# Optimization experiments

Measured on AMD Instinct MI355X. Metric: run time of the kernel, lower is better.

The kernel has to match this reference:

```python
import jax, jax.numpy as jnp
import numpy as np

EPS = 1e-5

def spmm(rows, cols, vals, x, n_out):
    # COO sparse [n_out, n_in] @ x [n_in, d] -> [n_out, d]
    return jax.ops.segment_sum(vals[:, None] * x[cols], rows, num_segments=n_out)

def layernorm(x, g, b):
    mu = jnp.mean(x, axis=-1, keepdims=True)
    var = jnp.var(x, axis=-1, keepdims=True)
    return (x - mu) * jax.lax.rsqrt(var + EPS) * g + b

def setup_inputs() -> dict:
    key = jax.random.key(0)
    ks = jax.random.split(key, 32)
    N, D = 100000, 512
    N0, N1, N2 = 131072, 32768, 8192
    E_s0, E_s1 = 262144, 65536
    E_f0, E_f1 = 1048576, 262144
    s = 1.0 / np.sqrt(D)
    inp = {
        'x': jax.random.normal(ks[0], (N, D), jnp.float32),
        'hist0': jax.random.normal(ks[1], (N, D), jnp.float32),
        'hist1': jax.random.normal(ks[2], (N, D), jnp.float32),
        'w0': jax.random.normal(ks[3], (D, D), jnp.float32) * s,
        'b0': jax.random.normal(ks[4], (D,), jnp.float32) * s,
        'g0': jnp.ones((D,), jnp.float32),
        'beta0': jnp.zeros((D,), jnp.float32),
        'w1': jax.random.normal(ks[5], (D, D), jnp.float32) * s,
        'b1': jax.random.normal(ks[6], (D,), jnp.float32) * s,
        'sadj0_vals': jax.random.uniform(ks[7], (E_s0,), jnp.float32),
        'sadj1_vals': jax.random.uniform(ks[8], (E_s1,), jnp.float32),
        'fadj0_vals': jax.random.uniform(ks[9], (E_f0,), jnp.float32),
        'fadj1_vals': jax.random.uniform(ks[10], (E_f1,), jnp.float32),
        'sid0': jax.random.randint(ks[11], (N0,), 0, N),
        'sid1': jax.random.randint(ks[12], (N1,), 0, N),
        'sid2': jax.random.randint(ks[13], (N2,), 0, N),
        'fid0': jax.random.randint(ks[14], (N0,), 0, N),
        'fid1': jax.random.randint(ks[15], (N1,), 0, N),
        'sadj0_rows': jax.random.randint(ks[16], (E_s0,), 0, N1),
        'sadj0_cols': jax.random.randint(ks[17], (E_s0,), 0, N0),
        'sadj1_rows': jax.random.randint(ks[18], (E_s1,), 0, N2),
        'sadj1_cols': jax.random.randint(ks[19], (E_s1,), 0, N1),
        'fadj0_rows': jax.random.randint(ks[20], (E_f0,), 0, N1),
        'fadj0_cols': jax.random.randint(ks[21], (E_f0,), 0, N0),
        'fadj1_rows': jax.random.randint(ks[22], (E_f1,), 0, N2),
        'fadj1_cols': jax.random.randint(ks[23], (E_f1,), 0, N1),
    }
    return inp

def reference(x, hist0, hist1, w0, b0, g0, beta0, w1, b1,
              sadj0_vals, sadj1_vals, fadj0_vals, fadj1_vals,
              sid0, sid1, sid2, fid0, fid1,
              sadj0_rows, sadj0_cols, sadj1_rows, sadj1_cols,
              fadj0_rows, fadj0_cols, fadj1_rows, fadj1_cols):
    N1 = sid1.shape[0]
    N2 = sid2.shape[0]
    sg = jax.lax.stop_gradient
    # layer 0
    h = x[sid0]                                   # [N0, D]
    h = h - sg(hist0[sid0])                        # variance-reduction correction
    full = sg(spmm(fadj0_rows, fadj0_cols, fadj0_vals, hist0[fid0], N1))
    h = spmm(sadj0_rows, sadj0_cols, sadj0_vals, h, N1) + full  # [N1, D]
    h = h @ w0.T + b0
    h = jax.nn.relu(layernorm(h, g0, beta0))
    # layer 1 (last: no norm/relu)
    h = h - sg(hist1[sid1])
    full = sg(spmm(fadj1_rows, fadj1_cols, fadj1_vals, hist1[fid1], N2))
    h = spmm(sadj1_rows, sadj1_cols, sadj1_vals, h, N2) + full  # [N2, D]
    h = h @ w1.T + b1
    return jax.nn.log_softmax(h, axis=-1)
```

## Files before the change

### kernel.cpp

```cpp
#include <hip/hip_runtime.h>

#define D 512
#define NTAB 100000

typedef __bf16 bf16x8 __attribute__((ext_vector_type(8)));
typedef float f32x4 __attribute__((ext_vector_type(4)));
typedef float f32x2 __attribute__((ext_vector_type(2)));

__device__ __forceinline__ unsigned f2bf(float f){
  union { float f; unsigned u; } v; v.f = f;
  unsigned r = v.u + 0x7fffu + ((v.u >> 16) & 1u);
  return r >> 16;
}
__device__ __forceinline__ float bf2f(unsigned h){
  union { unsigned u; float f; } v; v.u = h << 16; return v.f;
}
__device__ __forceinline__ uint2 enc_fp8x8(f32x4 v0, f32x4 v1){
  int lo = __builtin_amdgcn_cvt_pk_fp8_f32(v0[0], v0[1], 0, false);
  lo     = __builtin_amdgcn_cvt_pk_fp8_f32(v0[2], v0[3], lo, true);
  int hi = __builtin_amdgcn_cvt_pk_fp8_f32(v1[0], v1[1], 0, false);
  hi     = __builtin_amdgcn_cvt_pk_fp8_f32(v1[2], v1[3], hi, true);
  return make_uint2((unsigned)lo, (unsigned)hi);
}

#define MA_NS   6400
#define MA_GRID (MA_NS*9 + 512)

__global__ __launch_bounds__(256) void k_megaA(
    const int* __restrict__ s0r, int nS0,
    const int* __restrict__ f0r, int nF0, int* __restrict__ cnt0,
    const int* __restrict__ s1r, int nS1, int* __restrict__ cnt_s1,
    const int* __restrict__ f1r, int nF1, int* __restrict__ cnt_f1,
    const float* __restrict__ x, const float* __restrict__ hist0,
    unsigned char* __restrict__ T0q,
    const float* __restrict__ w0, const float* __restrict__ w1,
    unsigned short* __restrict__ w0b, unsigned short* __restrict__ w1b)
{
  int b = blockIdx.x, t = threadIdx.x;
  if (b < MA_NS*9){
    int sb = b / 9, r = b % 9;
    if (r == 0){
      int i = sb*256 + t;
      if (i < nS0){ atomicAdd(&cnt0[s0r[i]], 2); return; }
      i -= nS0;
      if (i < nF0){ atomicAdd(&cnt0[f0r[i]], 1); return; }
      i -= nF0;
      if (i < nS1){ atomicAdd(&cnt_s1[s1r[i]], 1); return; }
      i -= nS1;
      atomicAdd(&cnt_f1[f1r[i]], 1);
      return;
    }
    int ci = (sb*8 + (r-1))*256 + t;
    const int PER = NTAB*D/8;
    if (ci >= 2*PER) return;
    const float* src = (ci < PER) ? x : hist0;
    int ii = (ci < PER) ? ci : ci - PER;
    const f32x4* p = (const f32x4*)(src + (size_t)ii*8);
    f32x4 v0 = __builtin_nontemporal_load(p);
    f32x4 v1 = __builtin_nontemporal_load(p+1);
    *(uint2*)(T0q + (size_t)ci*8) = enc_fp8x8(v0, v1);
  } else {
    int i = (b - MA_NS*9)*256 + t;
    const float* src = (i < 65536) ? w0 : w1;
    unsigned short* dst = (i < 65536) ? w0b : w1b;
    int ii = (i < 65536) ? i : i - 65536;
    f32x4 v = *(const f32x4*)(src + (size_t)ii*4);
    ushort4 o;
    o.x = (unsigned short)f2bf(v[0]); o.y = (unsigned short)f2bf(v[1]);
    o.z = (unsigned short)f2bf(v[2]); o.w = (unsigned short)f2bf(v[3]);
    *(ushort4*)(dst + (size_t)ii*4) = o;
  }
}

__global__ __launch_bounds__(1024) void k_exscan3(
    const int* c0, int* r0, int n0,
    const int* c1, int* r1, int n1,
    const int* c2, int* r2, int n2)
{
  __shared__ int part[1024];
  const int* cnt; int* rp; int n;
  switch (blockIdx.x){
    case 0: cnt=c0; rp=r0; n=n0; break;
    case 1: cnt=c1; rp=r1; n=n1; break;
    default: cnt=c2; rp=r2; n=n2; break;
  }
  int t = threadIdx.x;
  int chunk = n >> 10;
  int base = t*chunk;
  int s = 0;
  for (int i=0;i<chunk;i++) s += cnt[base+i];
  part[t] = s; __syncthreads();
  for (int off=1; off<1024; off<<=1){
    int v = (t>=off) ? part[t-off] : 0;
    __syncthreads();
    part[t] += v;
    __syncthreads();
  }
  int run = (t==0) ? 0 : part[t-1];
  for (int i=0;i<chunk;i++){ rp[base+i] = run; run += cnt[base+i]; }
  if (t == 1023) rp[n] = run;
}

#define MB_NS   6554
#define MB_GRID (MB_NS*6)

__global__ __launch_bounds__(256) void k_megaB(
    const int* __restrict__ s0r, const int* __restrict__ s0c, const float* __restrict__ s0v, int nS0,
    const int* __restrict__ f0r, const int* __restrict__ f0c, const float* __restrict__ f0v, int nF0,
    const int* __restrict__ sid0, const int* __restrict__ fid0,
    const int* __restrict__ rp0, int* __restrict__ fill0, int2* __restrict__ bce0,
    const int* __restrict__ s1r, const int* __restrict__ s1c, const float* __restrict__ s1v, int nS1,
    const int* __restrict__ rp_s1, int* __restrict__ fill_s1, int2* __restrict__ bce_s1,
    const int* __restrict__ f1r, const int* __restrict__ f1c, const float* __restrict__ f1v, int nF1,
    const int* __restrict__ rp_f1, int* __restrict__ fill_f1, int2* __restrict__ bce_f1,
    const float* __restrict__ hist1, const int* __restrict__ fid1, const int* __restrict__ sid1,
    unsigned short* __restrict__ g1buf, unsigned short* __restrict__ s1buf)
{
  int b = blockIdx.x, t = threadIdx.x;
  int sb = b / 6, r = b % 6;
  if (r == 0){
    if (sb >= 6400) return;
    int i = sb*256 + t;
    if (i < nS0){
      int rr = s0r[i];
      int p = atomicAdd(&fill0[rr], 2);
      int base = rp0[rr] + p;
      int c = sid0[s0c[i]];
      float v = s0v[i];
      bce0[base]   = make_int2(c,        __float_as_int(v));
      bce0[base+1] = make_int2(NTAB + c, __float_as_int(-v));
      return;
    }
    i -= nS0;
    if (i < nF0){
      int rr = f0r[i];
      int p = atomicAdd(&fill0[rr], 1);
      bce0[rp0[rr] + p] = make_int2(NTAB + fid0[f0c[i]], __float_as_int(f0v[i]));
      return;
    }
    i -= nF0;
    if (i < nS1){
      int rr = s1r[i];
      int p = atomicAdd(&fill_s1[rr], 1);
      bce_s1[rp_s1[rr] + p] = make_int2(s1c[i], __float_as_int(s1v[i]));
      return;
    }
    i -= nS1;
    {
      int rr = f1r[i];
      int p = atomicAdd(&fill_f1[rr], 1);
      bce_f1[rp_f1[rr] + p] = make_int2(f1c[i], __float_as_int(f1v[i]));
    }
  } else {
    int g = sb*5 + (r-1);
    if (g >= 32768) return;
    const int* idx = (g < 16384) ? fid1 : sid1;
    unsigned short* dst = (g < 16384) ? g1buf : s1buf;
    if (g >= 16384) g -= 16384;
    int gt = g*256 + t;
    int row = gt >> 7, q = (gt & 127) << 2;
    int s = idx[row];
    f32x4 v = __builtin_nontemporal_load((const f32x4*)(hist1 + (size_t)s*D + q));
    ushort4 o;
    o.x = (unsigned short)f2bf(v[0]); o.y = (unsigned short)f2bf(v[1]);
    o.z = (unsigned short)f2bf(v[2]); o.w = (unsigned short)f2bf(v[3]);
    *(ushort4*)(dst + (size_t)row*D + q) = o;
  }
}

__device__ __forceinline__ void acc_bf16(float* a, uint4 p, float v){
  a[0] += v*bf2f(p.x & 0xffffu); a[1] += v*bf2f(p.x >> 16);
  a[2] += v*bf2f(p.y & 0xffffu); a[3] += v*bf2f(p.y >> 16);
  a[4] += v*bf2f(p.z & 0xffffu); a[5] += v*bf2f(p.z >> 16);
  a[6] += v*bf2f(p.w & 0xffffu); a[7] += v*bf2f(p.w >> 16);
}
__device__ __forceinline__ void acc_fp8(float* a, uint2 q, float v){
  f32x2 d0 = __builtin_amdgcn_cvt_pk_f32_fp8(q.x, false);
  f32x2 d1 = __builtin_amdgcn_cvt_pk_f32_fp8(q.x, true);
  f32x2 d2 = __builtin_amdgcn_cvt_pk_f32_fp8(q.y, false);
  f32x2 d3 = __builtin_amdgcn_cvt_pk_f32_fp8(q.y, true);
  a[0] += v*d0[0]; a[1] += v*d0[1]; a[2] += v*d1[0]; a[3] += v*d1[1];
  a[4] += v*d2[0]; a[5] += v*d2[1]; a[6] += v*d3[0]; a[7] += v*d3[1];
}

__device__ __forceinline__ void spmm_phase(
    const int* __restrict__ rp, const int2* __restrict__ be,
    const unsigned short* __restrict__ H, int row, int lane, float* a)
{
  int j = rp[row], je = rp[row+1];
  for (; j + 8 <= je; j += 8){
    int2 e[8]; uint4 p[8];
    #pragma unroll
    for (int u=0;u<8;u++) e[u] = be[j+u];
    #pragma unroll
    for (int u=0;u<8;u++) p[u] = *(const uint4*)(H + (size_t)e[u].x*D + lane*8);
    #pragma unroll
    for (int u=0;u<8;u++) acc_bf16(a, p[u], __int_as_float(e[u].y));
  }
  if (j + 4 <= je){
    int2 e[4]; uint4 p[4];
    #pragma unroll
    for (int u=0;u<4;u++) e[u] = be[j+u];
    #pragma unroll
    for (int u=0;u<4;u++) p[u] = *(const uint4*)(H + (size_t)e[u].x*D + lane*8);
    #pragma unroll
    for (int u=0;u<4;u++) acc_bf16(a, p[u], __int_as_float(e[u].y));
    j += 4;
  }
  for (; j < je; j++){
    int2 e = be[j];
    uint4 p = *(const uint4*)(H + (size_t)e.x*D + lane*8);
    acc_bf16(a, p, __int_as_float(e.y));
  }
}

__device__ __forceinline__ void spmm_phase_q8(
    const int* __restrict__ rp, const int2* __restrict__ be,
    const unsigned char* __restrict__ Q, int row, int lane, float* a)
{
  int j = rp[row], je = rp[row+1];
  for (; j + 8 <= je; j += 8){
    int2 e[8]; uint2 q[8];
    #pragma unroll
    for (int u=0;u<8;u++) e[u] = be[j+u];
    #pragma unroll
    for (int u=0;u<8;u++) q[u] = *(const uint2*)(Q + (size_t)e[u].x*D + lane*8);
    #pragma unroll
    for (int u=0;u<8;u++) acc_fp8(a, q[u], __int_as_float(e[u].y));
  }
  if (j + 4 <= je){
    int2 e[4]; uint2 q[4];
    #pragma unroll
    for (int u=0;u<4;u++) e[u] = be[j+u];
    #pragma unroll
    for (int u=0;u<4;u++) q[u] = *(const uint2*)(Q + (size_t)e[u].x*D + lane*8);
    #pragma unroll
    for (int u=0;u<4;u++) acc_fp8(a, q[u], __int_as_float(e[u].y));
    j += 4;
  }
  for (; j < je; j++){
    int2 e = be[j];
    uint2 q = *(const uint2*)(Q + (size_t)e.x*D + lane*8);
    acc_fp8(a, q, __int_as_float(e.y));
  }
}

__device__ __forceinline__ void store_row(unsigned short* out, int row, int lane, const float* a){
  uint4 o;
  o.x = f2bf(a[0]) | (f2bf(a[1]) << 16);
  o.y = f2bf(a[2]) | (f2bf(a[3]) << 16);
  o.z = f2bf(a[4]) | (f2bf(a[5]) << 16);
  o.w = f2bf(a[6]) | (f2bf(a[7]) << 16);
  *(uint4*)(out + (size_t)row*D + lane*8) = o;
}

__global__ __launch_bounds__(256) void k_spmm0(
    const int* __restrict__ rp, const int2* __restrict__ be,
    const unsigned char* __restrict__ T0q,
    unsigned short* __restrict__ out, int nrows)
{
  int wid = threadIdx.x >> 6, lane = threadIdx.x & 63;
  int row = blockIdx.x*4 + wid;
  if (row >= nrows) return;
  float a[8] = {0.f,0.f,0.f,0.f,0.f,0.f,0.f,0.f};
  spmm_phase_q8(rp, be, T0q, row, lane, a);
  store_row(out, row, lane, a);
}

__global__ __launch_bounds__(256) void k_spmm_acc(
    const int* __restrict__ rp, const int2* __restrict__ be, const unsigned short* __restrict__ H,
    unsigned short* __restrict__ out, int nrows)
{
  int wid = threadIdx.x >> 6, lane = threadIdx.x & 63;
  int row = blockIdx.x*4 + wid;
  if (row >= nrows) return;
  float a[8];
  uint4 p = *(const uint4*)(out + (size_t)row*D + lane*8);
  a[0]=bf2f(p.x&0xffffu); a[1]=bf2f(p.x>>16); a[2]=bf2f(p.y&0xffffu); a[3]=bf2f(p.y>>16);
  a[4]=bf2f(p.z&0xffffu); a[5]=bf2f(p.z>>16); a[6]=bf2f(p.w&0xffffu); a[7]=bf2f(p.w>>16);
  spmm_phase(rp, be, H, row, lane, a);
  store_row(out, row, lane, a);
}

__device__ __forceinline__ void gload16(const unsigned short* g, unsigned short* l){
  __builtin_amdgcn_global_load_lds(
      (const __attribute__((address_space(1))) unsigned int*)(const void*)g,
      (__attribute__((address_space(3))) unsigned int*)(void*)l,
      16, 0, 0);
}

template<bool OUT_BF16>
__device__ __forceinline__ void gemm_block(
    const unsigned short* __restrict__ A,
    const unsigned short* __restrict__ B,
    const float* __restrict__ bias,
    void* __restrict__ Cv,
    int gemm_bid, unsigned short* Al, unsigned short* Bl)
{
  int bx = gemm_bid & 3, by = gemm_bid >> 2;
  int m0 = by << 7, n0 = bx << 7;
  int t = threadIdx.x, wave = t >> 6, lane = t & 63;
  int wr = wave >> 1, wc = wave & 1;
  f32x4 acc[4][4] = {};
  int flat = t << 3;
  int r0 = flat >> 5, cc = flat & 31;
  const unsigned short* pa = A + (size_t)(m0 + r0)*D + cc;
  const unsigned short* pb = B + (size_t)(n0 + r0)*D + cc;
  for (int k0 = 0; k0 < D; k0 += 32){
    gload16(pa + k0,                 &Al[flat]);
    gload16(pa + (size_t)64*D + k0,  &Al[flat + 2048]);
    gload16(pb + k0,                 &Bl[flat]);
    gload16(pb + (size_t)64*D + k0,  &Bl[flat + 2048]);
    __syncthreads();
    int arow = (wr << 6) | (lane & 15);
    int brow = (wc << 6) | (lane & 15);
    int kg   = (lane >> 4) << 3;
    bf16x8 af[4], bfr[4];
    #pragma unroll
    for (int mi=0; mi<4; mi++) af[mi]  = *(const bf16x8*)&Al[(arow + (mi<<4))*32 + kg];
    #pragma unroll
    for (int ni=0; ni<4; ni++) bfr[ni] = *(const bf16x8*)&Bl[(brow + (ni<<4))*32 + kg];
    #pragma unroll
    for (int mi=0; mi<4; mi++)
      #pragma unroll
      for (int ni=0; ni<4; ni++)
        acc[mi][ni] = __builtin_amdgcn_mfma_f32_16x16x32_bf16(af[mi], bfr[ni], acc[mi][ni], 0, 0, 0);
    __syncthreads();
  }
  int crow = m0 + (wr << 6) + ((lane >> 4) << 2);
  int ccol = n0 + (wc << 6) + (lane & 15);
  #pragma unroll
  for (int mi=0; mi<4; mi++){
    #pragma unroll
    for (int q=0; q<4; q++){
      int row = crow + (mi << 4) + q;
      #pragma unroll
      for (int ni=0; ni<4; ni++){
        float val = acc[mi][ni][q] + bias[ccol + (ni << 4)];
        if (OUT_BF16)
          ((unsigned short*)Cv)[(size_t)row*D + ccol + (ni << 4)] = (unsigned short)f2bf(val);
        else
          ((float*)Cv)[(size_t)row*D + ccol + (ni << 4)] = val;
      }
    }
  }
}

__global__ __launch_bounds__(256) void k_megaC(
    const unsigned short* __restrict__ A, const unsigned short* __restrict__ B,
    const float* __restrict__ bias, unsigned short* __restrict__ y1,
    const int* __restrict__ rpf, const int2* __restrict__ bef,
    const unsigned short* __restrict__ g1buf, unsigned short* __restrict__ out2, int n2rows)
{
  __shared__ unsigned short Al[128*32];
  __shared__ unsigned short Bl[128*32];
  int b = blockIdx.x, t = threadIdx.x;
  int sb = b / 3, r = b % 3;
  if (r == 0){
    gemm_block<true>(A, B, bias, (void*)y1, sb, Al, Bl);
  } else {
    int wid = t >> 6, lane = t & 63;
    int row = (sb*2 + (r-1))*4 + wid;
    if (row >= n2rows) return;
    float a[8] = {0.f,0.f,0.f,0.f,0.f,0.f,0.f,0.f};
    spmm_phase(rpf, bef, g1buf, row, lane, a);
    store_row(out2, row, lane, a);
  }
}

template<bool OUT_BF16>
__global__ __launch_bounds__(256) void k_gemm_bias(
    const unsigned short* __restrict__ A,
    const unsigned short* __restrict__ B,
    const float* __restrict__ bias,
    void* __restrict__ Cv,
    int M)
{
  __shared__ unsigned short Al[128*32];
  __shared__ unsigned short Bl[128*32];
  gemm_block<OUT_BF16>(A, B, bias, Cv, blockIdx.x, Al, Bl);
}

__global__ __launch_bounds__(256) void k_ln_relu_sub(
    const unsigned short* __restrict__ y, const float* __restrict__ gam, const float* __restrict__ bet,
    const unsigned short* __restrict__ s1buf, unsigned short* __restrict__ out)
{
  __shared__ float sh[8];
  int row = blockIdx.x, t = threadIdx.x;
  int c = t << 1;
  unsigned pv = *(const unsigned*)(y + (size_t)row*D + c);
  float vx = bf2f(pv & 0xffffu), vy = bf2f(pv >> 16);
  float s = vx + vy, ss = vx*vx + vy*vy;
  #pragma unroll
  for (int m=1; m<64; m<<=1){ s += __shfl_xor(s, m); ss += __shfl_xor(ss, m); }
  int wave = t >> 6, lane = t & 63;
  if (lane == 0){ sh[wave] = s; sh[4+wave] = ss; }
  __syncthreads();
  s  = sh[0]+sh[1]+sh[2]+sh[3];
  ss = sh[4]+sh[5]+sh[6]+sh[7];
  float mu  = s * (1.f/D);
  float var = ss * (1.f/D) - mu*mu;
  float rr  = rsqrtf(var + 1e-5f);
  unsigned hv = *(const unsigned*)(s1buf + (size_t)row*D + c);
  float o0 = fmaxf((vx - mu)*rr*gam[c]   + bet[c],   0.f) - bf2f(hv & 0xffffu);
  float o1 = fmaxf((vy - mu)*rr*gam[c+1] + bet[c+1], 0.f) - bf2f(hv >> 16);
  *(unsigned*)(out + (size_t)row*D + c) = f2bf(o0) | (f2bf(o1) << 16);
}

__global__ __launch_bounds__(256) void k_logsoftmax(const float* __restrict__ y, float* __restrict__ out){
  __shared__ float sh[8];
  int row = blockIdx.x, t = threadIdx.x;
  int c = t << 1;
  float2 v = *(const float2*)(y + (size_t)row*D + c);
  float m = fmaxf(v.x, v.y);
  #pragma unroll
  for (int k=1; k<64; k<<=1) m = fmaxf(m, __shfl_xor(m, k));
  int wave = t >> 6, lane = t & 63;
  if (lane == 0) sh[wave] = m;
  __syncthreads();
  m = fmaxf(fmaxf(sh[0], sh[1]), fmaxf(sh[2], sh[3]));
  __syncthreads();
  float e = expf(v.x - m) + expf(v.y - m);
  #pragma unroll
  for (int k=1; k<64; k<<=1) e += __shfl_xor(e, k);
  if (lane == 0) sh[4+wave] = e;
  __syncthreads();
  e = sh[4]+sh[5]+sh[6]+sh[7];
  float lse = m + logf(e);
  float2 o; o.x = v.x - lse; o.y = v.y - lse;
  *(float2*)(out + (size_t)row*D + c) = o;
}

extern "C" void kernel_launch(void* const* d_in, const int* in_sizes, int n_in,
                              void* d_out, int out_size, void* d_ws, size_t ws_size,
                              hipStream_t stream)
{
  const float* x     = (const float*)d_in[0];
  const float* hist0 = (const float*)d_in[1];
  const float* hist1 = (const float*)d_in[2];
  const float* w0    = (const float*)d_in[3];
  const float* b0    = (const float*)d_in[4];
  const float* g0    = (const float*)d_in[5];
  const float* beta0 = (const float*)d_in[6];
  const float* w1    = (const float*)d_in[7];
  const float* b1    = (const float*)d_in[8];
  const float* s0v   = (const float*)d_in[9];
  const float* s1v   = (const float*)d_in[10];
  const float* f0v   = (const float*)d_in[11];
  const float* f1v   = (const float*)d_in[12];
  const int* sid0    = (const int*)d_in[13];
  const int* sid1    = (const int*)d_in[14];
  const int* fid0    = (const int*)d_in[16];
  const int* fid1    = (const int*)d_in[17];
  const int* s0r     = (const int*)d_in[18];
  const int* s0c     = (const int*)d_in[19];
  const int* s1r     = (const int*)d_in[20];
  const int* s1c     = (const int*)d_in[21];
  const int* f0r     = (const int*)d_in[22];
  const int* f0c     = (const int*)d_in[23];
  const int* f1r     = (const int*)d_in[24];
  const int* f1c     = (const int*)d_in[25];

  const int N1 = 32768, N2 = 8192;
  const int Es0 = 262144, Es1 = 65536, Ef0 = 1048576, Ef1 = 262144;
  const int E0 = 2*Es0 + Ef0;

  char* ws = (char*)d_ws;
  size_t off = 0;
  auto alloc = [&](size_t bytes)->char*{
    char* p = ws + off; off += (bytes + 255) & ~(size_t)255; return p;
  };
  char* T0q_raw = alloc((size_t)2*NTAB*D);
  unsigned short* g1buf = (unsigned short*)alloc((size_t)N1*D*2);
  unsigned short* s1buf = (unsigned short*)alloc((size_t)N1*D*2);
  unsigned short* h1    = (unsigned short*)alloc((size_t)N1*D*2);
  unsigned short* out1  = (unsigned short*)alloc((size_t)N1*D*2);
  unsigned short* w0b   = (unsigned short*)alloc((size_t)D*D*2);
  unsigned short* w1b   = (unsigned short*)alloc((size_t)D*D*2);
  int* meta = (int*)alloc((size_t)(2*N1 + 4*N2)*4);
  int* cnt0   = meta;            int* fill0   = cnt0 + N1;
  int* cnt_s1 = fill0 + N1;      int* fill_s1 = cnt_s1 + N2;
  int* cnt_f1 = fill_s1 + N2;    int* fill_f1 = cnt_f1 + N2;
  size_t metaBytes = (size_t)(2*N1 + 4*N2)*4;
  int* rp0   = (int*)alloc((size_t)(N1+1)*4);
  int* rp_s1 = (int*)alloc((size_t)(N2+1)*4);
  int* rp_f1 = (int*)alloc((size_t)(N2+1)*4);
  int2* bce0   = (int2*)alloc((size_t)E0*8);
  int2* bce_s1 = (int2*)alloc((size_t)Es1*8);
  int2* bce_f1 = (int2*)alloc((size_t)Ef1*8);

  unsigned char*  T0q  = (unsigned char*)T0q_raw;
  unsigned short* y1   = (unsigned short*)T0q_raw;
  float*          y2   = (float*)(T0q_raw + ((size_t)34<<20));
  unsigned short* out2 = (unsigned short*)(T0q_raw + ((size_t)52<<20));
  float*          outp = (float*)d_out;

  hipMemsetAsync(meta, 0, metaBytes, stream);
  k_megaA<<<MA_GRID, 256, 0, stream>>>(
      s0r, Es0, f0r, Ef0, cnt0, s1r, Es1, cnt_s1, f1r, Ef1, cnt_f1,
      x, hist0, T0q, w0, w1, w0b, w1b);
  k_exscan3<<<3, 1024, 0, stream>>>(cnt0, rp0, N1, cnt_s1, rp_s1, N2, cnt_f1, rp_f1, N2);
  k_megaB<<<MB_GRID, 256, 0, stream>>>(
      s0r, s0c, s0v, Es0, f0r, f0c, f0v, Ef0, sid0, fid0, rp0, fill0, bce0,
      s1r, s1c, s1v, Es1, rp_s1, fill_s1, bce_s1,
      f1r, f1c, f1v, Ef1, rp_f1, fill_f1, bce_f1,
      hist1, fid1, sid1, g1buf, s1buf);
  k_spmm0<<<N1/4, 256, 0, stream>>>(rp0, bce0, T0q, out1, N1);
  k_megaC<<<1024*3, 256, 0, stream>>>(out1, w0b, b0, y1, rp_f1, bce_f1, g1buf, out2, N2);
  k_ln_relu_sub<<<N1, 256, 0, stream>>>(y1, g0, beta0, s1buf, h1);
  k_spmm_acc<<<N2/4, 256, 0, stream>>>(rp_s1, bce_s1, h1, out2, N2);
  k_gemm_bias<false><<<(N2/128)*4, 256, 0, stream>>>(out2, w1b, b1, (void*)y2, N2);
  k_logsoftmax<<<N2, 256, 0, stream>>>(y2, outp);
}
```

Measured before the change: 549.7 us.

## Quantize full hist1 table to fp8 and index it directly instead of gathering bf16 copies

hist1 is now converted whole into an fp8 table (H1q) inside the first mega kernel, replacing the per-row bf16 gathers into g1buf/s1buf. The fill kernel now stores fid1 indices in the f1 CSR entries, and the layernorm kernel reads H1q through sid1. This removes the separate gather-and-convert pass and shrinks the bytes read in the second-layer spmm and the subtraction. In exchange it converts all 100k rows of hist1 rather than only the 64k gathered ones, and fp8 loses precision compared with bf16. Numeric tolerance may be at risk.

```diff
diff --git a/kernel.cpp b/kernel.cpp
--- a/kernel.cpp
+++ b/kernel.cpp
@@ -24,21 +24,22 @@
 }
 
 #define MA_NS   6400
-#define MA_GRID (MA_NS*9 + 512)
+#define MA_GRID (MA_NS*13 + 512)
+#define PER8    (NTAB*D/8)
 
 __global__ __launch_bounds__(256) void k_megaA(
     const int* __restrict__ s0r, int nS0,
     const int* __restrict__ f0r, int nF0, int* __restrict__ cnt0,
     const int* __restrict__ s1r, int nS1, int* __restrict__ cnt_s1,
     const int* __restrict__ f1r, int nF1, int* __restrict__ cnt_f1,
-    const float* __restrict__ x, const float* __restrict__ hist0,
-    unsigned char* __restrict__ T0q,
+    const float* __restrict__ x, const float* __restrict__ hist0, const float* __restrict__ hist1,
+    unsigned char* __restrict__ T0q, unsigned char* __restrict__ H1q,
     const float* __restrict__ w0, const float* __restrict__ w1,
     unsigned short* __restrict__ w0b, unsigned short* __restrict__ w1b)
 {
   int b = blockIdx.x, t = threadIdx.x;
-  if (b < MA_NS*9){
-    int sb = b / 9, r = b % 9;
+  if (b < MA_NS*13){
+    int sb = b / 13, r = b % 13;
     if (r == 0){
       int i = sb*256 + t;
       if (i < nS0){ atomicAdd(&cnt0[s0r[i]], 2); return; }
@@ -50,17 +51,28 @@
       atomicAdd(&cnt_f1[f1r[i]], 1);
       return;
     }
-    int ci = (sb*8 + (r-1))*256 + t;
-    const int PER = NTAB*D/8;
-    if (ci >= 2*PER) return;
-    const float* src = (ci < PER) ? x : hist0;
-    int ii = (ci < PER) ? ci : ci - PER;
-    const f32x4* p = (const f32x4*)(src + (size_t)ii*8);
-    f32x4 v0 = __builtin_nontemporal_load(p);
-    f32x4 v1 = __builtin_nontemporal_load(p+1);
-    *(uint2*)(T0q + (size_t)ci*8) = enc_fp8x8(v0, v1);
+    if (r < 9){
+      int ci = (sb*8 + (r-1))*256 + t;
+      if (ci >= 2*PER8) return;
+      const float* src = (ci < PER8) ? x : hist0;
+      int ii = (ci < PER8) ? ci : ci - PER8;
+      const f32x4* p = (const f32x4*)(src + (size_t)ii*8);
+      f32x4 v0 = __builtin_nontemporal_load(p);
+      f32x4 v1 = __builtin_nontemporal_load(p+1);
+      *(uint2*)(T0q + (size_t)ci*8) = enc_fp8x8(v0, v1);
+      return;
+    }
+    {
+      int ci = (sb*4 + (r-9))*256 + t;
+      if (ci >= PER8) return;
+      const f32x4* p = (const f32x4*)(hist1 + (size_t)ci*8);
+      f32x4 v0 = __builtin_nontemporal_load(p);
+      f32x4 v1 = __builtin_nontemporal_load(p+1);
+      *(uint2*)(H1q + (size_t)ci*8) = enc_fp8x8(v0, v1);
+      return;
+    }
   } else {
-    int i = (b - MA_NS*9)*256 + t;
+    int i = (b - MA_NS*13)*256 + t;
     const float* src = (i < 65536) ? w0 : w1;
     unsigned short* dst = (i < 65536) ? w0b : w1b;
     int ii = (i < 65536) ? i : i - 65536;
@@ -101,70 +113,49 @@
   if (t == 1023) rp[n] = run;
 }
 
-#define MB_NS   6554
-#define MB_GRID (MB_NS*6)
-
-__global__ __launch_bounds__(256) void k_megaB(
+__global__ __launch_bounds__(256) void k_fill(
     const int* __restrict__ s0r, const int* __restrict__ s0c, const float* __restrict__ s0v, int nS0,
     const int* __restrict__ f0r, const int* __restrict__ f0c, const float* __restrict__ f0v, int nF0,
     const int* __restrict__ sid0, const int* __restrict__ fid0,
     const int* __restrict__ rp0, int* __restrict__ fill0, int2* __restrict__ bce0,
     const int* __restrict__ s1r, const int* __restrict__ s1c, const float* __restrict__ s1v, int nS1,
     const int* __restrict__ rp_s1, int* __restrict__ fill_s1, int2* __restrict__ bce_s1,
-    const int* __restrict__ f1r, const int* __restrict__ f1c, const float* __restrict__ f1v, int nF1,
-    const int* __restrict__ rp_f1, int* __restrict__ fill_f1, int2* __restrict__ bce_f1,
-    const float* __restrict__ hist1, const int* __restrict__ fid1, const int* __restrict__ sid1,
-    unsigned short* __restrict__ g1buf, unsigned short* __restrict__ s1buf)
-{
-  int b = blockIdx.x, t = threadIdx.x;
-  int sb = b / 6, r = b % 6;
-  if (r == 0){
-    if (sb >= 6400) return;
-    int i = sb*256 + t;
-    if (i < nS0){
-      int rr = s0r[i];
-      int p = atomicAdd(&fill0[rr], 2);
-      int base = rp0[rr] + p;
-      int c = sid0[s0c[i]];
-      float v = s0v[i];
-      bce0[base]   = make_int2(c,        __float_as_int(v));
-      bce0[base+1] = make_int2(NTAB + c, __float_as_int(-v));
-      return;
-    }
-    i -= nS0;
-    if (i < nF0){
-      int rr = f0r[i];
-      int p = atomicAdd(&fill0[rr], 1);
-      bce0[rp0[rr] + p] = make_int2(NTAB + fid0[f0c[i]], __float_as_int(f0v[i]));
-      return;
-    }
-    i -= nF0;
-    if (i < nS1){
-      int rr = s1r[i];
-      int p = atomicAdd(&fill_s1[rr], 1);
-      bce_s1[rp_s1[rr] + p] = make_int2(s1c[i], __float_as_int(s1v[i]));
-      return;
-    }
-    i -= nS1;
-    {
-      int rr = f1r[i];
-      int p = atomicAdd(&fill_f1[rr], 1);
-      bce_f1[rp_f1[rr] + p] = make_int2(f1c[i], __float_as_int(f1v[i]));
-    }
-  } else {
-    int g = sb*5 + (r-1);
-    if (g >= 32768) return;
-    const int* idx = (g < 16384) ? fid1 : sid1;
-    unsigned short* dst = (g < 16384) ? g1buf : s1buf;
-    if (g >= 16384) g -= 16384;
-    int gt = g*256 + t;
-    int row = gt >> 7, q = (gt & 127) << 2;
-    int s = idx[row];
-    f32x4 v = __builtin_nontemporal_load((const f32x4*)(hist1 + (size_t)s*D + q));
-    ushort4 o;
-    o.x = (unsigned short)f2bf(v[0]); o.y = (unsigned short)f2bf(v[1]);
-    o.z = (unsigned short)f2bf(v[2]); o.w = (unsigned short)f2bf(v[3]);
-    *(ushort4*)(dst + (size_t)row*D + q) = o;
+    const int* __restrict__ f1r, const int* __restrict__ f1c, const float* __restrict__ f1v,
+    const int* __restrict__ fid1,
+    const int* __restrict__ rp_f1, int* __restrict__ fill_f1, int2* __restrict__ bce_f1)
+{
+  int i = blockIdx.x*256 + threadIdx.x;
+  if (i < nS0){
+    int rr = s0r[i];
+    int c  = sid0[s0c[i]];
+    float v = s0v[i];
+    int p = atomicAdd(&fill0[rr], 2);
+    int base = rp0[rr] + p;
+    bce0[base]   = make_int2(c,        __float_as_int(v));
+    bce0[base+1] = make_int2(NTAB + c, __float_as_int(-v));
+    return;
+  }
+  i -= nS0;
+  if (i < nF0){
+    int rr = f0r[i];
+    int c  = NTAB + fid0[f0c[i]];
+    int p = atomicAdd(&fill0[rr], 1);
+    bce0[rp0[rr] + p] = make_int2(c, __float_as_int(f0v[i]));
+    return;
+  }
+  i -= nF0;
+  if (i < nS1){
+    int rr = s1r[i];
+    int p = atomicAdd(&fill_s1[rr], 1);
+    bce_s1[rp_s1[rr] + p] = make_int2(s1c[i], __float_as_int(s1v[i]));
+    return;
+  }
+  i -= nS1;
+  {
+    int rr = f1r[i];
+    int c  = fid1[f1c[i]];
+    int p = atomicAdd(&fill_f1[rr], 1);
+    bce_f1[rp_f1[rr] + p] = make_int2(c, __float_as_int(f1v[i]));
   }
 }
 
@@ -350,7 +341,7 @@
     const unsigned short* __restrict__ A, const unsigned short* __restrict__ B,
     const float* __restrict__ bias, unsigned short* __restrict__ y1,
     const int* __restrict__ rpf, const int2* __restrict__ bef,
-    const unsigned short* __restrict__ g1buf, unsigned short* __restrict__ out2, int n2rows)
+    const unsigned char* __restrict__ H1q, unsigned short* __restrict__ out2, int n2rows)
 {
   __shared__ unsigned short Al[128*32];
   __shared__ unsigned short Bl[128*32];
@@ -363,7 +354,7 @@
     int row = (sb*2 + (r-1))*4 + wid;
     if (row >= n2rows) return;
     float a[8] = {0.f,0.f,0.f,0.f,0.f,0.f,0.f,0.f};
-    spmm_phase(rpf, bef, g1buf, row, lane, a);
+    spmm_phase_q8(rpf, bef, H1q, row, lane, a);
     store_row(out2, row, lane, a);
   }
 }
@@ -381,9 +372,10 @@
   gemm_block<OUT_BF16>(A, B, bias, Cv, blockIdx.x, Al, Bl);
 }
 
-__global__ __launch_bounds__(256) void k_ln_relu_sub(
+__global__ __launch_bounds__(256) void k_ln_relu_subq(
     const unsigned short* __restrict__ y, const float* __restrict__ gam, const float* __restrict__ bet,
-    const unsigned short* __restrict__ s1buf, unsigned short* __restrict__ out)
+    const unsigned char* __restrict__ H1q, const int* __restrict__ sid1,
+    unsigned short* __restrict__ out)
 {
   __shared__ float sh[8];
   int row = blockIdx.x, t = threadIdx.x;
@@ -401,9 +393,11 @@
   float mu  = s * (1.f/D);
   float var = ss * (1.f/D) - mu*mu;
   float rr  = rsqrtf(var + 1e-5f);
-  unsigned hv = *(const unsigned*)(s1buf + (size_t)row*D + c);
-  float o0 = fmaxf((vx - mu)*rr*gam[c]   + bet[c],   0.f) - bf2f(hv & 0xffffu);
-  float o1 = fmaxf((vy - mu)*rr*gam[c+1] + bet[c+1], 0.f) - bf2f(hv >> 16);
+  int srow = sid1[row];
+  unsigned short qv = *(const unsigned short*)(H1q + (size_t)srow*D + c);
+  f32x2 d = __builtin_amdgcn_cvt_pk_f32_fp8((unsigned)qv, false);
+  float o0 = fmaxf((vx - mu)*rr*gam[c]   + bet[c],   0.f) - d[0];
+  float o1 = fmaxf((vy - mu)*rr*gam[c+1] + bet[c+1], 0.f) - d[1];
   *(unsigned*)(out + (size_t)row*D + c) = f2bf(o0) | (f2bf(o1) << 16);
 }
 
@@ -471,12 +465,11 @@
     char* p = ws + off; off += (bytes + 255) & ~(size_t)255; return p;
   };
   char* T0q_raw = alloc((size_t)2*NTAB*D);
-  unsigned short* g1buf = (unsigned short*)alloc((size_t)N1*D*2);
-  unsigned short* s1buf = (unsigned short*)alloc((size_t)N1*D*2);
-  unsigned short* h1    = (unsigned short*)alloc((size_t)N1*D*2);
-  unsigned short* out1  = (unsigned short*)alloc((size_t)N1*D*2);
-  unsigned short* w0b   = (unsigned short*)alloc((size_t)D*D*2);
-  unsigned short* w1b   = (unsigned short*)alloc((size_t)D*D*2);
+  unsigned char* H1q = (unsigned char*)alloc((size_t)NTAB*D);
+  unsigned short* h1   = (unsigned short*)alloc((size_t)N1*D*2);
+  unsigned short* out1 = (unsigned short*)alloc((size_t)N1*D*2);
+  unsigned short* w0b  = (unsigned short*)alloc((size_t)D*D*2);
+  unsigned short* w1b  = (unsigned short*)alloc((size_t)D*D*2);
   int* meta = (int*)alloc((size_t)(2*N1 + 4*N2)*4);
   int* cnt0   = meta;            int* fill0   = cnt0 + N1;
   int* cnt_s1 = fill0 + N1;      int* fill_s1 = cnt_s1 + N2;
@@ -498,16 +491,15 @@
   hipMemsetAsync(meta, 0, metaBytes, stream);
   k_megaA<<<MA_GRID, 256, 0, stream>>>(
       s0r, Es0, f0r, Ef0, cnt0, s1r, Es1, cnt_s1, f1r, Ef1, cnt_f1,
-      x, hist0, T0q, w0, w1, w0b, w1b);
+      x, hist0, hist1, T0q, H1q, w0, w1, w0b, w1b);
   k_exscan3<<<3, 1024, 0, stream>>>(cnt0, rp0, N1, cnt_s1, rp_s1, N2, cnt_f1, rp_f1, N2);
-  k_megaB<<<MB_GRID, 256, 0, stream>>>(
+  k_fill<<<6400, 256, 0, stream>>>(
       s0r, s0c, s0v, Es0, f0r, f0c, f0v, Ef0, sid0, fid0, rp0, fill0, bce0,
       s1r, s1c, s1v, Es1, rp_s1, fill_s1, bce_s1,
-      f1r, f1c, f1v, Ef1, rp_f1, fill_f1, bce_f1,
-      hist1, fid1, sid1, g1buf, s1buf);
+      f1r, f1c, f1v, fid1, rp_f1, fill_f1, bce_f1);
   k_spmm0<<<N1/4, 256, 0, stream>>>(rp0, bce0, T0q, out1, N1);
-  k_megaC<<<1024*3, 256, 0, stream>>>(out1, w0b, b0, y1, rp_f1, bce_f1, g1buf, out2, N2);
-  k_ln_relu_sub<<<N1, 256, 0, stream>>>(y1, g0, beta0, s1buf, h1);
+  k_megaC<<<1024*3, 256, 0, stream>>>(out1, w0b, b0, y1, rp_f1, bce_f1, H1q, out2, N2);
+  k_ln_relu_subq<<<N1, 256, 0, stream>>>(y1, g0, beta0, H1q, sid1, h1);
   k_spmm_acc<<<N2/4, 256, 0, stream>>>(rp_s1, bce_s1, h1, out2, N2);
   k_gemm_bias<false><<<(N2/128)*4, 256, 0, stream>>>(out2, w1b, b1, (void*)y2, N2);
   k_logsoftmax<<<N2, 256, 0, stream>>>(y2, outp);
```

After: 528.7 us. -3.8%, faster.
